# Optimization experiments

Measured on AMD Instinct MI355X. Metric: run time of the kernel, lower is better.

Reference implementation:

```python
import jax, jax.numpy as jnp
import numpy as np

EMBED_DIM = 1024
ATTN_DIM = 1024


def setup_inputs() -> dict:
    key = jax.random.key(0)
    k1, k2, k3, k4 = jax.random.split(key, 4)
    embedded = jax.random.normal(k1, (4, 2048, EMBED_DIM), dtype=jnp.float32)
    # torch nn.Linear weights are [out_features, in_features]
    s = 1.0 / np.sqrt(EMBED_DIM)
    Wk = jax.random.uniform(k2, (ATTN_DIM, EMBED_DIM), jnp.float32, -s, s)
    Wq = jax.random.uniform(k3, (ATTN_DIM, EMBED_DIM), jnp.float32, -s, s)
    Wv = jax.random.uniform(k4, (ATTN_DIM, EMBED_DIM), jnp.float32, -s, s)
    return {"embedded": embedded, "Wk": Wk, "Wq": Wq, "Wv": Wv}


def reference(embedded, Wk, Wq, Wv):
    # projections: x @ W.T  (torch Linear, no bias)
    k = jnp.einsum("bse,ae->bsa", embedded, Wk)
    q = jnp.einsum("bse,ae->bsa", embedded, Wq)
    v = jnp.einsum("bse,ae->bsa", embedded, Wv)
    scale = 1.0 / jnp.sqrt(jnp.float32(ATTN_DIM))
    attn = jnp.einsum("bqa,bka->bqk", q, k) * scale  # [B, S, S]
    S = attn.shape[1]
    causal = jnp.tril(jnp.ones((S, S), dtype=bool))
    attn = jnp.where(causal[None, :, :], attn, -jnp.inf)
    a = jax.nn.softmax(attn, axis=2)
    out = jnp.einsum("bqk,bka->bqa", a, v)
    return jnp.round(out, 4)
```

## Files before the change

kernel.cpp:

```cpp
#include <hip/hip_runtime.h>
#include <hip/hip_bf16.h>
#include <hip/hip_fp16.h>
#include <stdint.h>

typedef __bf16 bf16_t;
typedef bf16_t bf16x8 __attribute__((ext_vector_type(8)));
typedef bf16_t bf16x4 __attribute__((ext_vector_type(4)));
typedef float f32x4 __attribute__((ext_vector_type(4)));

#define BM 128
#define BN 128
#define BK 32

__device__ __forceinline__ void gload_lds16(const void* g, void* l) {
    __builtin_amdgcn_global_load_lds(
        (const __attribute__((address_space(1))) void*)(uintptr_t)g,
        (__attribute__((address_space(3))) void*)(uintptr_t)l,
        16, 0, 0);
}

template <int EPI>
__device__ __forceinline__ void gemm_body(
    bf16_t* __restrict__ As, bf16_t* __restrict__ Bs,
    const bf16_t* __restrict__ A, long lda,
    const bf16_t* __restrict__ B, long ldb,
    void* __restrict__ Cv, long ldc,
    int k0beg, int k1end, float scale, int m0, int n0,
    float* __restrict__ rs)
{
    const int tid = threadIdx.x;
    const int wid = tid >> 6, lane = tid & 63;
    const int wr = wid >> 1, wc = wid & 1;
    const int hw = lane >> 4, ln = lane & 15;

    const bf16_t *srcA[2], *srcB[2];
#pragma unroll
    for (int i = 0; i < 2; i++) {
        const int c = tid + i * 256;
        const int row = c >> 2;
        const int j = ((c & 3) - (row >> 1)) & 3;
        srcA[i] = A + (size_t)(m0 + row) * lda + j * 8;
        srcB[i] = B + (size_t)(n0 + row) * ldb + j * 8;
    }

    f32x4 acc[4][4] = {};

    for (int k0 = k0beg; k0 < k1end; k0 += BK) {
        gload_lds16(srcA[0] + k0, &As[wid * 512]);
        gload_lds16(srcA[1] + k0, &As[2048 + wid * 512]);
        gload_lds16(srcB[0] + k0, &Bs[wid * 512]);
        gload_lds16(srcB[1] + k0, &Bs[2048 + wid * 512]);
        __syncthreads();

        bf16x8 af[4], bfr[4];
#pragma unroll
        for (int t = 0; t < 4; t++) {
            const int r  = wr * 64 + t * 16 + ln;
            const int rb = wc * 64 + t * 16 + ln;
            af[t]  = *(const bf16x8*)&As[r  * BK + (((hw + (r  >> 1)) & 3) * 8)];
            bfr[t] = *(const bf16x8*)&Bs[rb * BK + (((hw + (rb >> 1)) & 3) * 8)];
        }
#pragma unroll
        for (int ti = 0; ti < 4; ti++)
#pragma unroll
            for (int tj = 0; tj < 4; tj++)
                acc[ti][tj] = __builtin_amdgcn_mfma_f32_16x16x32_bf16(
                    af[ti], bfr[tj], acc[ti][tj], 0, 0, 0);
        __syncthreads();
    }

#pragma unroll
    for (int ti = 0; ti < 4; ti++) {
        const int rbase = m0 + wr * 64 + ti * 16 + hw * 4;
        f32x4 inv4;
        if (EPI == 2) {
            const float4 r4 = *(const float4*)&rs[rbase];
            inv4[0] = 1.0f / r4.x; inv4[1] = 1.0f / r4.y;
            inv4[2] = 1.0f / r4.z; inv4[3] = 1.0f / r4.w;
        }
        float part[4] = {0.f, 0.f, 0.f, 0.f};
#pragma unroll
        for (int tj = 0; tj < 4; tj++) {
            const int col = n0 + wc * 64 + tj * 16 + ln;
            if (EPI == 4) {
                const int bb = rbase >> 11;
                const int s  = rbase & 2047;
                const int d  = col - 2048;
                bf16x4 o;
#pragma unroll
                for (int rg = 0; rg < 4; rg++) o[rg] = (bf16_t)acc[ti][tj][rg];
                *(bf16x4*)&((bf16_t*)Cv)[(size_t)bb * 2097152 + (size_t)d * 2048 + s] = o;
            } else {
#pragma unroll
                for (int rg = 0; rg < 4; rg++) {
                    const size_t idx = (size_t)(rbase + rg) * ldc + col;
                    if (EPI == 0) {
                        ((bf16_t*)Cv)[idx] = (bf16_t)(acc[ti][tj][rg]);
                    } else if (EPI == 2) {
                        ((float*)Cv)[idx] = acc[ti][tj][rg] * inv4[rg];
                    } else {
                        const float e = (col <= rbase + rg)
                                      ? __expf(acc[ti][tj][rg] * scale) : 0.0f;
                        part[rg] += e;
                        ((bf16_t*)Cv)[idx] = (bf16_t)e;
                    }
                }
            }
        }
        if (EPI == 3) {
#pragma unroll
            for (int rg = 0; rg < 4; rg++) {
                float p = part[rg];
                p += __shfl_xor(p, 1, 64);
                p += __shfl_xor(p, 2, 64);
                p += __shfl_xor(p, 4, 64);
                p += __shfl_xor(p, 8, 64);
                if (ln == 0) atomicAdd(&rs[rbase + rg], p);
            }
        }
    }
}

__global__ __launch_bounds__(256) void gemm1_qkv(
    const bf16_t* __restrict__ xb, const bf16_t* __restrict__ Wb,
    bf16_t* __restrict__ QKVb, bf16_t* __restrict__ Vt)
{
    __shared__ __align__(16) bf16_t As[BM * BK];
    __shared__ __align__(16) bf16_t Bs[BN * BK];
    const int lin = blockIdx.x;
    const int xcd = lin & 7;
    const int j   = lin >> 3;
    const int p   = j >> 6;
    const int w   = j & 63;
    const int mblk = xcd * 8 + (w >> 3);
    const int nblk = p * 8 + (w & 7);
    const int m0 = mblk * BM, n0 = nblk * BN;
    if (nblk < 16)
        gemm_body<0>(As, Bs, xb, 1024, Wb, 1024, QKVb, 2048,
                     0, 1024, 1.0f, m0, n0, nullptr);
    else
        gemm_body<4>(As, Bs, xb, 1024, Wb, 1024, Vt, 2048,
                     0, 1024, 1.0f, m0, n0, nullptr);
}

__global__ __launch_bounds__(256) void qk_gemm(
    const bf16_t* __restrict__ QKVb, bf16_t* __restrict__ E,
    float* __restrict__ rowsum)
{
    __shared__ __align__(16) bf16_t As[BM * BK];
    __shared__ __align__(16) bf16_t Bs[BN * BK];
    const int b = blockIdx.x & 3;
    int rem = blockIdx.x >> 2;
    int my = 15, nx = 0;
#pragma unroll
    for (int m = 15; m >= 0; --m) {
        if (rem < m + 1) { my = m; nx = rem; break; }
        rem -= m + 1;
    }
    const bf16_t* base = QKVb + (size_t)b * (2048L * 2048);
    gemm_body<3>(As, Bs,
                 base + 1024, 2048,
                 base, 2048,
                 E + (size_t)b * (2048L * 2048), 2048,
                 0, 1024, 0.03125f, my * BM, nx * BN,
                 rowsum + b * 2048);
}

__global__ __launch_bounds__(256) void gemm3_pv(
    const bf16_t* __restrict__ E, const bf16_t* __restrict__ Vt,
    const float* __restrict__ rowsum, float* __restrict__ out)
{
    __shared__ __align__(16) bf16_t As[BM * BK];
    __shared__ __align__(16) bf16_t Bs[BN * BK];
    const int id = blockIdx.x;
    const int strip = 15 - (id >> 5);
    const int nx = (id >> 2) & 7;
    const int b = id & 3;
    const int m0 = strip * BM;
    gemm_body<2>(As, Bs,
                 E + (size_t)b * (2048L * 2048), 2048,
                 Vt + (size_t)b * (1024L * 2048), 2048,
                 out + (size_t)b * (2048L * 1024), 1024,
                 0, m0 + BM, 1.0f, m0, nx * BN,
                 (float*)rowsum + b * 2048);
}

__global__ __launch_bounds__(256) void cast_all(
    const float* __restrict__ x,
    const float* __restrict__ Wk, const float* __restrict__ Wq,
    const float* __restrict__ Wv,
    bf16_t* __restrict__ xb, bf16_t* __restrict__ Wb,
    float* __restrict__ rowsum)
{
    const int blk = blockIdx.x;
    if (blk >= 11264) {
        const size_t i = ((size_t)(blk - 11264) * 256 + threadIdx.x) * 4;
        *(float4*)(rowsum + i) = make_float4(0.f, 0.f, 0.f, 0.f);
        return;
    }
    const float* src;
    bf16_t* dst;
    if (blk < 8192) {
        const size_t i = ((size_t)blk * 256 + threadIdx.x) * 4;
        src = x + i;
        dst = xb + i;
    } else {
        const size_t j = ((size_t)(blk - 8192) * 256 + threadIdx.x) * 4;
        dst = Wb + j;
        if (j < (size_t)1048576)      src = Wk + j;
        else if (j < (size_t)2097152) src = Wq + (j - 1048576);
        else                          src = Wv + (j - 2097152);
    }
    const float4 v = *(const float4*)src;
    bf16x4 o;
    o.x = (bf16_t)v.x; o.y = (bf16_t)v.y; o.z = (bf16_t)v.z; o.w = (bf16_t)v.w;
    *(bf16x4*)dst = o;
}

extern "C" void kernel_launch(void* const* d_in, const int* in_sizes, int n_in,
                              void* d_out, int out_size, void* d_ws, size_t ws_size,
                              hipStream_t stream)
{
    const float* x  = (const float*)d_in[0];
    const float* Wk = (const float*)d_in[1];
    const float* Wq = (const float*)d_in[2];
    const float* Wv = (const float*)d_in[3];
    char* ws = (char*)d_ws;

    bf16_t* QKVb   = (bf16_t*)(ws);
    bf16_t* Vt     = (bf16_t*)(ws + ((size_t)32 << 20));
    bf16_t* xb     = (bf16_t*)(ws + ((size_t)48 << 20));
    bf16_t* Wb     = (bf16_t*)(ws + ((size_t)64 << 20));
    bf16_t* E      = (bf16_t*)(ws + ((size_t)48 << 20));
    float*  rowsum = (float*)(ws + ((size_t)80 << 20));
    float*  out    = (float*)d_out;

    cast_all<<<11272, 256, 0, stream>>>(x, Wk, Wq, Wv, xb, Wb, rowsum);

    gemm1_qkv<<<1536, 256, 0, stream>>>(xb, Wb, QKVb, Vt);

    qk_gemm<<<544, 256, 0, stream>>>(QKVb, E, rowsum);

    gemm3_pv<<<512, 256, 0, stream>>>(E, Vt, rowsum, out);
}
```

Before: 226.0 us.

## Rewrite QKV projection GEMM as 256x256 tile, double-buffered, phase-scheduled kernel

Replaces the 128x128 single-buffered QKV projection GEMM with a 512-thread 256x256 tile kernel that uses BK=64, a double-buffered 128KB LDS, and prefetching two k-steps ahead. The MFMA work is split into four quadrant phases interleaved with global-to-LDS loads, using explicit barriers, waitcnt and setprio. The aim is to raise data reuse per tile and hide global load latency behind matrix math. The cost is fewer blocks (384), more fragile hand scheduling, and a ring-index wrap (kt & (nt-1)) that assumes nt is a power of two.

```diff
diff --git a/kernel.cpp b/kernel.cpp
--- a/kernel.cpp
+++ b/kernel.cpp
@@ -82,28 +82,16 @@
 #pragma unroll
         for (int tj = 0; tj < 4; tj++) {
             const int col = n0 + wc * 64 + tj * 16 + ln;
-            if (EPI == 4) {
-                const int bb = rbase >> 11;
-                const int s  = rbase & 2047;
-                const int d  = col - 2048;
-                bf16x4 o;
-#pragma unroll
-                for (int rg = 0; rg < 4; rg++) o[rg] = (bf16_t)acc[ti][tj][rg];
-                *(bf16x4*)&((bf16_t*)Cv)[(size_t)bb * 2097152 + (size_t)d * 2048 + s] = o;
-            } else {
-#pragma unroll
-                for (int rg = 0; rg < 4; rg++) {
-                    const size_t idx = (size_t)(rbase + rg) * ldc + col;
-                    if (EPI == 0) {
-                        ((bf16_t*)Cv)[idx] = (bf16_t)(acc[ti][tj][rg]);
-                    } else if (EPI == 2) {
-                        ((float*)Cv)[idx] = acc[ti][tj][rg] * inv4[rg];
-                    } else {
-                        const float e = (col <= rbase + rg)
-                                      ? __expf(acc[ti][tj][rg] * scale) : 0.0f;
-                        part[rg] += e;
-                        ((bf16_t*)Cv)[idx] = (bf16_t)e;
-                    }
+#pragma unroll
+            for (int rg = 0; rg < 4; rg++) {
+                const size_t idx = (size_t)(rbase + rg) * ldc + col;
+                if (EPI == 2) {
+                    ((float*)Cv)[idx] = acc[ti][tj][rg] * inv4[rg];
+                } else {
+                    const float e = (col <= rbase + rg)
+                                  ? __expf(acc[ti][tj][rg] * scale) : 0.0f;
+                    part[rg] += e;
+                    ((bf16_t*)Cv)[idx] = (bf16_t)e;
                 }
             }
         }
@@ -121,26 +109,182 @@
     }
 }
 
-__global__ __launch_bounds__(256) void gemm1_qkv(
+template <int EPI>
+__device__ __forceinline__ void gemm256_body(
+    bf16_t* __restrict__ lds,
+    const bf16_t* __restrict__ A, long lda,
+    const bf16_t* __restrict__ B, long ldb,
+    void* __restrict__ Cv, long ldc,
+    int nt, int m0, int n0)
+{
+    const int tid = threadIdx.x;
+    const int wid = tid >> 6, lane = tid & 63;
+    const int wr = wid >> 2, wcn = wid & 3;
+    const int hw = lane >> 4, ln = lane & 15;
+
+    const int srow = (wid << 3) + (lane >> 3);
+    const int clog = ((lane & 7) - (lane >> 3)) & 7;
+    const bf16_t* sA = A + (size_t)(m0 + srow) * lda + clog * 8;
+    const bf16_t* sB = B + (size_t)(n0 + srow) * ldb + clog * 8;
+    char* ldsc = (char*)lds;
+    const int wb = wid << 10;
+
+#define STG_A(bf, q, kt) gload_lds16(sA + (size_t)(q) * 64 * lda + (size_t)(kt) * 64, \
+                                     ldsc + (bf) * 65536 + (q) * 8192 + wb)
+#define STG_B(bf, q, kt) gload_lds16(sB + (size_t)(q) * 64 * ldb + (size_t)(kt) * 64, \
+                                     ldsc + (bf) * 65536 + 32768 + (q) * 8192 + wb)
+
+    const int c0 = ((hw + ln) & 7) << 4;
+    const int c1 = ((hw + ln + 4) & 7) << 4;
+    const int aR = (wr * 128 + ln) * 128;
+    const int bR = 32768 + (wcn * 64 + ln) * 128;
+
+#define RDA(bf, fr, ks) (*(const bf16x8*)(ldsc + (bf) * 65536 + aR + (fr) * 2048 + ((ks) ? c1 : c0)))
+#define RDB(bf, fc, ks) (*(const bf16x8*)(ldsc + (bf) * 65536 + bR + (fc) * 2048 + ((ks) ? c1 : c0)))
+
+    f32x4 acc[8][4] = {};
+
+    STG_A(0, 0, 0); STG_A(0, 2, 0); STG_B(0, 0, 0); STG_B(0, 1, 0);
+    STG_A(0, 1, 0); STG_A(0, 3, 0); STG_B(0, 2, 0); STG_B(0, 3, 0);
+    STG_A(1, 0, 1); STG_A(1, 2, 1); STG_B(1, 0, 1); STG_B(1, 1, 1);
+    STG_A(1, 1, 1); STG_A(1, 3, 1);
+    asm volatile("s_waitcnt vmcnt(6)" ::: "memory");
+    __builtin_amdgcn_s_barrier();
+
+    for (int t = 0; t < nt; ++t) {
+        const int bc = t & 1, bn = bc ^ 1;
+        const int kt1 = (t + 1) & (nt - 1);
+        const int kt2 = (t + 2) & (nt - 1);
+        bf16x8 af[4][2], bl[2][2], bh[2][2];
+
+#pragma unroll
+        for (int fr = 0; fr < 4; ++fr) {
+            af[fr][0] = RDA(bc, fr, 0);
+            af[fr][1] = RDA(bc, fr, 1);
+        }
+#pragma unroll
+        for (int fc = 0; fc < 2; ++fc) {
+            bl[fc][0] = RDB(bc, fc, 0);
+            bl[fc][1] = RDB(bc, fc, 1);
+        }
+        STG_B(bn, 2, kt1); STG_B(bn, 3, kt1);
+        __builtin_amdgcn_s_barrier();
+        asm volatile("s_waitcnt lgkmcnt(0)" ::: "memory");
+        __builtin_amdgcn_sched_barrier(0);
+        __builtin_amdgcn_s_setprio(1);
+#pragma unroll
+        for (int fr = 0; fr < 4; ++fr)
+#pragma unroll
+            for (int fc = 0; fc < 2; ++fc)
+#pragma unroll
+                for (int ks = 0; ks < 2; ++ks)
+                    acc[fr][fc] = __builtin_amdgcn_mfma_f32_16x16x32_bf16(
+                        af[fr][ks], bl[fc][ks], acc[fr][fc], 0, 0, 0);
+        __builtin_amdgcn_s_setprio(0);
+        __builtin_amdgcn_s_barrier();
+
+#pragma unroll
+        for (int fc = 0; fc < 2; ++fc) {
+            bh[fc][0] = RDB(bc, fc + 2, 0);
+            bh[fc][1] = RDB(bc, fc + 2, 1);
+        }
+        STG_A(bc, 0, kt2); STG_A(bc, 2, kt2);
+        __builtin_amdgcn_s_barrier();
+        asm volatile("s_waitcnt lgkmcnt(0)" ::: "memory");
+        __builtin_amdgcn_sched_barrier(0);
+        __builtin_amdgcn_s_setprio(1);
+#pragma unroll
+        for (int fr = 0; fr < 4; ++fr)
+#pragma unroll
+            for (int fc = 0; fc < 2; ++fc)
+#pragma unroll
+                for (int ks = 0; ks < 2; ++ks)
+                    acc[fr][fc + 2] = __builtin_amdgcn_mfma_f32_16x16x32_bf16(
+                        af[fr][ks], bh[fc][ks], acc[fr][fc + 2], 0, 0, 0);
+        __builtin_amdgcn_s_setprio(0);
+        __builtin_amdgcn_s_barrier();
+
+#pragma unroll
+        for (int fr = 0; fr < 4; ++fr) {
+            af[fr][0] = RDA(bc, fr + 4, 0);
+            af[fr][1] = RDA(bc, fr + 4, 1);
+        }
+        STG_B(bc, 0, kt2); STG_B(bc, 1, kt2);
+        __builtin_amdgcn_s_barrier();
+        asm volatile("s_waitcnt lgkmcnt(0)" ::: "memory");
+        __builtin_amdgcn_sched_barrier(0);
+        __builtin_amdgcn_s_setprio(1);
+#pragma unroll
+        for (int fr = 0; fr < 4; ++fr)
+#pragma unroll
+            for (int fc = 0; fc < 2; ++fc)
+#pragma unroll
+                for (int ks = 0; ks < 2; ++ks)
+                    acc[fr + 4][fc + 2] = __builtin_amdgcn_mfma_f32_16x16x32_bf16(
+                        af[fr][ks], bh[fc][ks], acc[fr + 4][fc + 2], 0, 0, 0);
+        __builtin_amdgcn_s_setprio(0);
+        __builtin_amdgcn_s_barrier();
+
+        STG_A(bc, 1, kt2); STG_A(bc, 3, kt2);
+        __builtin_amdgcn_s_setprio(1);
+#pragma unroll
+        for (int fr = 0; fr < 4; ++fr)
+#pragma unroll
+            for (int fc = 0; fc < 2; ++fc)
+#pragma unroll
+                for (int ks = 0; ks < 2; ++ks)
+                    acc[fr + 4][fc] = __builtin_amdgcn_mfma_f32_16x16x32_bf16(
+                        af[fr][ks], bl[fc][ks], acc[fr + 4][fc], 0, 0, 0);
+        __builtin_amdgcn_s_setprio(0);
+        asm volatile("s_waitcnt vmcnt(6)" ::: "memory");
+        __builtin_amdgcn_s_barrier();
+    }
+
+    asm volatile("s_waitcnt vmcnt(0)" ::: "memory");
+
+#pragma unroll
+    for (int fr = 0; fr < 8; ++fr) {
+        const int rbase = m0 + wr * 128 + fr * 16 + hw * 4;
+#pragma unroll
+        for (int fc = 0; fc < 4; ++fc) {
+            const int col = n0 + wcn * 64 + fc * 16 + ln;
+            if (EPI == 4) {
+                const int bb = rbase >> 11;
+                const int s  = rbase & 2047;
+                const int d  = col - 2048;
+                bf16x4 o;
+#pragma unroll
+                for (int rg = 0; rg < 4; rg++) o[rg] = (bf16_t)acc[fr][fc][rg];
+                *(bf16x4*)&((bf16_t*)Cv)[(size_t)bb * 2097152 + (size_t)d * 2048 + s] = o;
+            } else {
+#pragma unroll
+                for (int rg = 0; rg < 4; rg++)
+                    ((bf16_t*)Cv)[(size_t)(rbase + rg) * ldc + col] =
+                        (bf16_t)acc[fr][fc][rg];
+            }
+        }
+    }
+#undef STG_A
+#undef STG_B
+#undef RDA
+#undef RDB
+}
+
+__global__ __launch_bounds__(512, 2) void gemm1_qkv(
     const bf16_t* __restrict__ xb, const bf16_t* __restrict__ Wb,
     bf16_t* __restrict__ QKVb, bf16_t* __restrict__ Vt)
 {
-    __shared__ __align__(16) bf16_t As[BM * BK];
-    __shared__ __align__(16) bf16_t Bs[BN * BK];
+    __shared__ __align__(16) bf16_t lds[65536];
     const int lin = blockIdx.x;
     const int xcd = lin & 7;
     const int j   = lin >> 3;
-    const int p   = j >> 6;
-    const int w   = j & 63;
-    const int mblk = xcd * 8 + (w >> 3);
-    const int nblk = p * 8 + (w & 7);
-    const int m0 = mblk * BM, n0 = nblk * BN;
-    if (nblk < 16)
-        gemm_body<0>(As, Bs, xb, 1024, Wb, 1024, QKVb, 2048,
-                     0, 1024, 1.0f, m0, n0, nullptr);
+    const int mblk = xcd * 4 + (j & 3);
+    const int nblk = j >> 2;
+    const int m0 = mblk * 256, n0 = nblk * 256;
+    if (nblk < 8)
+        gemm256_body<0>(lds, xb, 1024, Wb, 1024, QKVb, 2048, 16, m0, n0);
     else
-        gemm_body<4>(As, Bs, xb, 1024, Wb, 1024, Vt, 2048,
-                     0, 1024, 1.0f, m0, n0, nullptr);
+        gemm256_body<4>(lds, xb, 1024, Wb, 1024, Vt, 2048, 16, m0, n0);
 }
 
 __global__ __launch_bounds__(256) void qk_gemm(
@@ -237,7 +381,7 @@
 
     cast_all<<<11272, 256, 0, stream>>>(x, Wk, Wq, Wv, xb, Wb, rowsum);
 
-    gemm1_qkv<<<1536, 256, 0, stream>>>(xb, Wb, QKVb, Vt);
+    gemm1_qkv<<<384, 512, 0, stream>>>(xb, Wb, QKVb, Vt);
 
     qk_gemm<<<544, 256, 0, stream>>>(QKVb, E, rowsum);
 
```

Result: no change. 229.2 us (+1.4%).
